# Performance work log

Hardware: AMD Instinct MI355X
Metric: run time of the kernel (lower is better)

Reference implementation:

```python
import jax, jax.numpy as jnp
import numpy as np

DIM = 192
NUM_HEADS = 4
B, H, W = 2, 256, 256
EPS = 1e-12  # torch F.normalize default eps


def setup_inputs() -> dict:
    key = jax.random.key(0)
    k1, k2, k3 = jax.random.split(key, 3)
    x = jax.random.normal(k1, (B, DIM, H, W), dtype=jnp.float32)
    # depthwise qkv conv: groups=DIM, each group maps 1 in-ch -> 3 out-ch; torch OIHW layout (3*DIM, 1, 3, 3)
    w_qkv = jax.random.normal(k2, (3 * DIM, 1, 3, 3), dtype=jnp.float32) * 0.1
    temperature = jnp.ones((NUM_HEADS, 1, 1), dtype=jnp.float32)
    # 1x1 projection conv, stored as [out, in]
    w_proj = jax.random.normal(k3, (DIM, DIM), dtype=jnp.float32) * (1.0 / np.sqrt(DIM))
    return {"x": x, "w_qkv": w_qkv, "temperature": temperature, "w_proj": w_proj}


def reference(x, w_qkv, temperature, w_proj):
    b, c, h, w = x.shape
    num_heads = temperature.shape[0]
    ch = c // num_heads  # channels per head
    # grouped (depthwise) 3x3 conv producing qkv; torch grouped-conv channel order
    # matches feature_group_count ordering (3 consecutive out-chs per group)... but
    # note torch chunk(3, dim=1) splits the 3*c output into contiguous thirds, so
    # q gets out-channels [0, c), etc. We replicate exactly with same layout.
    qkv = jax.lax.conv_general_dilated(
        x, w_qkv, window_strides=(1, 1), padding=((1, 1), (1, 1)),
        feature_group_count=c,
        dimension_numbers=("NCHW", "OIHW", "NCHW"))
    q, k, v = jnp.split(qkv, 3, axis=1)  # each [b, c, h, w]
    q = q.reshape(b, num_heads, ch, h * w)
    k = k.reshape(b, num_heads, ch, h * w)
    v = v.reshape(b, num_heads, ch, h * w)
    # L2 normalize along spatial dim (torch F.normalize with eps clamp)
    q = q / jnp.maximum(jnp.linalg.norm(q, axis=-1, keepdims=True), EPS)
    k = k / jnp.maximum(jnp.linalg.norm(k, axis=-1, keepdims=True), EPS)
    # channel-channel cosine attention, [b, head, ch, ch] (small)
    attn = jnp.einsum("bhcn,bhdn->bhcd", q, k) * temperature
    attn = jax.nn.softmax(attn, axis=-1)
    out = jnp.einsum("bhcd,bhdn->bhcn", attn, v).reshape(b, c, h, w)
    # 1x1 projection conv
    out = jnp.einsum("oi,bihw->bohw", w_proj, out)
    return out
```

## Files before the change

### kernel.cpp

```cpp
#include <hip/hip_runtime.h>
#include <math.h>

#define BB 2
#define CC 192
#define NH 4
#define CH 48
#define SRCP 16
#define HH 256
#define WW 256
#define NPIX (HH*WW)

typedef __attribute__((ext_vector_type(8))) short short8;
typedef __attribute__((ext_vector_type(4))) float f4;

static __device__ __forceinline__ unsigned short f2bf(float f) {
    union { float f; unsigned int u; } c; c.f = f;
    unsigned int r = c.u + 0x7fffu + ((c.u >> 16) & 1u);
    return (unsigned short)(r >> 16);
}

__global__ __launch_bounds__(256, 2) void k_conv(
    const float* __restrict__ x, const float* __restrict__ wqkv,
    unsigned short* __restrict__ vws, float* __restrict__ Sws,
    float* __restrict__ sqws)
{
    __shared__ float wlds[3*CH*9];
    __shared__ unsigned int qk32[2][CH][132];

    const int tid = threadIdx.x;
    const int hd = blockIdx.x;
    const int y  = blockIdx.y;
    const int b  = blockIdx.z;

    for (int i = tid; i < 3*CH*9; i += 256) {
        int type = i / (CH*9);
        int rem  = i - type*(CH*9);
        wlds[i] = wqkv[type*(CC*9) + hd*(CH*9) + rem];
    }
    __syncthreads();

    {
        const int xp = tid;
        const int y0 = (y > 0) ? (y-1) : 0;
        const int y2 = (y < HH-1) ? (y+1) : y;
        const int xl = (xp > 0) ? (xp-1) : 0;
        const int xr = (xp < WW-1) ? (xp+1) : xp;
        const float my0 = (y > 0) ? 1.f : 0.f;
        const float my2 = (y < HH-1) ? 1.f : 0.f;
        const float mx0 = (xp > 0) ? 1.f : 0.f;
        const float mx2 = (xp < WW-1) ? 1.f : 0.f;
        const float m00 = my0*mx0, m02 = my0*mx2, m20 = my2*mx0, m22 = my2*mx2;

        #pragma unroll
        for (int type = 0; type < 2; ++type) {
            const int srcbase = type*64 + SRCP*hd;
            const float* wt = &wlds[type*(CH*9)];
            for (int g = 0; g < SRCP; ++g) {
                const float* base = x + ((size_t)(b*CC + srcbase + g)*HH)*WW;
                const float* r0 = base + (size_t)y0*WW;
                const float* r1 = base + (size_t)y *WW;
                const float* r2 = base + (size_t)y2*WW;
                float a00 = r0[xl]*m00, a01 = r0[xp]*my0, a02 = r0[xr]*m02;
                float a10 = r1[xl]*mx0, a11 = r1[xp],     a12 = r1[xr]*mx2;
                float a20 = r2[xl]*m20, a21 = r2[xp]*my2, a22 = r2[xr]*m22;
                #pragma unroll
                for (int r = 0; r < 3; ++r) {
                    const int cl = 3*g + r;
                    const float* w = wt + cl*9;
                    float val = a00*w[0] + a01*w[1] + a02*w[2]
                              + a10*w[3] + a11*w[4] + a12*w[5]
                              + a20*w[6] + a21*w[7] + a22*w[8];
                    ((unsigned short*)&qk32[type][cl][0])[xp] = f2bf(val);
                }
            }
        }

        unsigned int vpack[24];
        {
            const int srcbase = 128 + SRCP*hd;
            const float* wt = &wlds[2*(CH*9)];
            #pragma unroll
            for (int g = 0; g < SRCP; ++g) {
                const float* base = x + ((size_t)(b*CC + srcbase + g)*HH)*WW;
                const float* r0 = base + (size_t)y0*WW;
                const float* r1 = base + (size_t)y *WW;
                const float* r2 = base + (size_t)y2*WW;
                float a00 = r0[xl]*m00, a01 = r0[xp]*my0, a02 = r0[xr]*m02;
                float a10 = r1[xl]*mx0, a11 = r1[xp],     a12 = r1[xr]*mx2;
                float a20 = r2[xl]*m20, a21 = r2[xp]*my2, a22 = r2[xr]*m22;
                #pragma unroll
                for (int r = 0; r < 3; ++r) {
                    const int cl = 3*g + r;
                    const float* w = wt + cl*9;
                    float val = a00*w[0] + a01*w[1] + a02*w[2]
                              + a10*w[3] + a11*w[4] + a12*w[5]
                              + a20*w[6] + a21*w[7] + a22*w[8];
                    unsigned int u = f2bf(val);
                    if (cl & 1) vpack[cl >> 1] |= (u << 16);
                    else        vpack[cl >> 1]  = u;
                }
            }
        }
        {
            unsigned short* vp = vws + ((size_t)b*NPIX + (size_t)y*WW + xp)*CC + hd*CH;
            #pragma unroll
            for (int st = 0; st < 6; ++st) {
                uint4 u; u.x = vpack[st*4+0]; u.y = vpack[st*4+1];
                         u.z = vpack[st*4+2]; u.w = vpack[st*4+3];
                *(uint4*)(vp + st*8) = u;
            }
        }
    }
    __syncthreads();

    if (tid < 2*CH) {
        const int which = tid / CH;
        const int cl = tid - which*CH;
        const uint4* row = (const uint4*)&qk32[which][cl][0];
        float ssum = 0.f;
        for (int j = 0; j < 32; ++j) {
            uint4 u = row[j];
            #pragma unroll
            for (int q4 = 0; q4 < 4; ++q4) {
                unsigned int w = (&u.x)[q4];
                float lo = __uint_as_float(w << 16);
                float hi = __uint_as_float(w & 0xffff0000u);
                ssum = fmaf(lo, lo, ssum);
                ssum = fmaf(hi, hi, ssum);
            }
        }
        atomicAdd(&sqws[((b*NH + hd)*2 + which)*CH + cl], ssum);
    }

    {
        const int lane = tid & 63;
        const int wv = tid >> 6;
        const int m = lane & 15, quad = lane >> 4;
        for (int p = wv; p < 9; p += 4) {
            const int ct = p / 3, dt = p - ct*3;
            f4 acc = {0.f, 0.f, 0.f, 0.f};
            const char* qbase = (const char*)&qk32[0][ct*16 + m][0] + quad*16;
            const char* kbase = (const char*)&qk32[1][dt*16 + m][0] + quad*16;
            #pragma unroll
            for (int ks = 0; ks < 8; ++ks) {
                short8 afr = *(const short8*)(qbase + ks*64);
                short8 bfr = *(const short8*)(kbase + ks*64);
                acc = __builtin_amdgcn_mfma_f32_16x16x32_bf16(afr, bfr, acc, 0, 0, 0);
            }
            const int c0 = ct*16 + quad*4, d = dt*16 + m;
            float* Sp = Sws + ((size_t)(b*NH + hd)*CH + c0)*CH + d;
            #pragma unroll
            for (int r = 0; r < 4; ++r) atomicAdd(Sp + r*CH, acc[r]);
        }
    }
}

__global__ __launch_bounds__(256) void k_attn(
    const float* __restrict__ Sws, const float* __restrict__ sqws,
    const float* __restrict__ temp, const float* __restrict__ wproj,
    unsigned short* __restrict__ W2bf)
{
    __shared__ float att[CH][CH+1];
    __shared__ float wp[CC][CH+1];
    __shared__ float nrm[2][CH];

    const int tid = threadIdx.x;
    const int b  = blockIdx.x >> 2;
    const int hd = blockIdx.x & 3;

    if (tid < 2*CH) {
        int which = tid / CH, cl = tid - which*CH;
        nrm[which][cl] = fmaxf(sqrtf(sqws[((b*NH + hd)*2 + which)*CH + cl]), 1e-12f);
    }
    __syncthreads();

    const float tscale = temp[hd];
    for (int m = tid; m < CH*CH; m += 256) {
        int c = m / CH, d = m - c*CH;
        att[c][d] = Sws[((size_t)(b*NH + hd)*CH + c)*CH + d] * tscale
                    / (nrm[0][c] * nrm[1][d]);
    }
    __syncthreads();

    if (tid < CH) {
        float mx = -1e30f;
        for (int d = 0; d < CH; ++d) mx = fmaxf(mx, att[tid][d]);
        float sm = 0.f;
        for (int d = 0; d < CH; ++d) { float e = expf(att[tid][d] - mx); att[tid][d] = e; sm += e; }
        float inv = 1.f / sm;
        for (int d = 0; d < CH; ++d) att[tid][d] *= inv;
    }

    for (int m = tid; m < CC*CH; m += 256) {
        int o = m / CH, il = m - o*CH;
        wp[o][il] = wproj[o*CC + hd*CH + il];
    }
    __syncthreads();

    const int o0  = (tid & 31) * 6;
    const int dl0 = (tid >> 5) * 6;
    float a[6][6];
    #pragma unroll
    for (int i = 0; i < 6; ++i)
        #pragma unroll
        for (int j = 0; j < 6; ++j) a[i][j] = 0.f;
    for (int il = 0; il < CH; ++il) {
        float wv[6], av[6];
        #pragma unroll
        for (int i = 0; i < 6; ++i) wv[i] = wp[o0+i][il];
        #pragma unroll
        for (int j = 0; j < 6; ++j) av[j] = att[il][dl0+j];
        #pragma unroll
        for (int i = 0; i < 6; ++i)
            #pragma unroll
            for (int j = 0; j < 6; ++j)
                a[i][j] = fmaf(wv[i], av[j], a[i][j]);
    }
    #pragma unroll
    for (int i = 0; i < 6; ++i)
        #pragma unroll
        for (int j = 0; j < 6; ++j)
            W2bf[((size_t)b*CC + o0 + i)*CC + hd*CH + dl0 + j] = f2bf(a[i][j]);
}

__global__ __launch_bounds__(256, 2) void k_out(
    const unsigned short* __restrict__ vws, const unsigned short* __restrict__ W2bf,
    float* __restrict__ out)
{
    __shared__ unsigned short w2l[CC][200];

    const int tid = threadIdx.x;
    const int b  = blockIdx.y;
    const int n0 = blockIdx.x * 128;

    {
        const uint4* src = (const uint4*)(W2bf + (size_t)b*CC*CC);
        for (int i = tid; i < CC*24; i += 256) {
            int o = i / 24, c = i - o*24;
            *(uint4*)&w2l[o][c*8] = src[i];
        }
    }
    __syncthreads();

    const int lane = tid & 63;
    const int wv = tid >> 6;
    const int m0  = (wv & 1) * 96;
    const int nn0 = (wv >> 1) * 64;
    const int m = lane & 15, quad = lane >> 4;

    f4 acc[6][4];
    #pragma unroll
    for (int mt = 0; mt < 6; ++mt)
        #pragma unroll
        for (int nt = 0; nt < 4; ++nt) acc[mt][nt] = (f4){0.f, 0.f, 0.f, 0.f};

    const unsigned short* vb = vws + ((size_t)b*NPIX + n0 + nn0 + m)*CC + quad*8;

    #pragma unroll
    for (int ks = 0; ks < 6; ++ks) {
        short8 bfr[4];
        #pragma unroll
        for (int nt = 0; nt < 4; ++nt)
            bfr[nt] = *(const short8*)(vb + (size_t)(nt*16)*CC + ks*32);
        short8 afr[6];
        #pragma unroll
        for (int mt = 0; mt < 6; ++mt)
            afr[mt] = *(const short8*)&w2l[m0 + mt*16 + m][ks*32 + quad*8];
        #pragma unroll
        for (int mt = 0; mt < 6; ++mt)
            #pragma unroll
            for (int nt = 0; nt < 4; ++nt)
                acc[mt][nt] = __builtin_amdgcn_mfma_f32_16x16x32_bf16(afr[mt], bfr[nt], acc[mt][nt], 0, 0, 0);
    }

    #pragma unroll
    for (int mt = 0; mt < 6; ++mt) {
        const int o = m0 + mt*16 + quad*4;
        #pragma unroll
        for (int nt = 0; nt < 4; ++nt) {
            const int px = n0 + nn0 + nt*16 + m;
            float* op = out + ((size_t)(b*CC + o))*NPIX + px;
            #pragma unroll
            for (int r = 0; r < 4; ++r) op[(size_t)r*NPIX] = acc[mt][nt][r];
        }
    }
}

extern "C" void kernel_launch(void* const* d_in, const int* in_sizes, int n_in,
                              void* d_out, int out_size, void* d_ws, size_t ws_size,
                              hipStream_t stream)
{
    const float* x     = (const float*)d_in[0];
    const float* wqkv  = (const float*)d_in[1];
    const float* temp  = (const float*)d_in[2];
    const float* wproj = (const float*)d_in[3];
    float* out = (float*)d_out;
    (void)in_sizes; (void)n_in; (void)out_size; (void)ws_size;

    unsigned short* vws = (unsigned short*)d_ws;
    const size_t VBYTES = (size_t)BB*CC*NPIX*sizeof(unsigned short);
    float* Sws  = (float*)((char*)d_ws + VBYTES);
    float* sqws = Sws + (size_t)BB*NH*CH*CH;
    unsigned short* W2bf = (unsigned short*)(sqws + (size_t)BB*NH*2*CH);

    hipMemsetAsync(Sws, 0, (size_t)(BB*NH*CH*CH + BB*NH*2*CH)*sizeof(float), stream);
    k_conv<<<dim3(NH, HH, BB), 256, 0, stream>>>(x, wqkv, vws, Sws, sqws);
    k_attn<<<dim3(BB*NH), 256, 0, stream>>>(Sws, sqws, temp, wproj, W2bf);
    k_out<<<dim3(NPIX/128, BB), 256, 0, stream>>>(vws, W2bf, out);
}
```

Before: 321.9 us.

## Split conv rows into half-width tiles with DPP neighbor exchange; drop LDS staging

The depthwise conv kernel now processes half a row per block, with the two thread halves covering different channel groups. Horizontal neighbors come from DPP lane shifts and readlane of halo values instead of three separate global loads per row. Weights are read straight from global memory rather than staged in LDS, and the output kernel reads W2 directly from global memory instead of copying it to LDS. This cuts redundant global loads and LDS footprint to raise occupancy, at the cost of twice as many atomic adds into the S accumulator and uncached weight reads.

```diff
diff --git a/kernel.cpp b/kernel.cpp
--- a/kernel.cpp
+++ b/kernel.cpp
@@ -5,7 +5,6 @@
 #define CC 192
 #define NH 4
 #define CH 48
-#define SRCP 16
 #define HH 256
 #define WW 256
 #define NPIX (HH*WW)
@@ -19,96 +18,107 @@
     return (unsigned short)(r >> 16);
 }
 
-__global__ __launch_bounds__(256, 2) void k_conv(
+template<int CTRL>
+static __device__ __forceinline__ float dppmv(float v) {
+    return __int_as_float(__builtin_amdgcn_update_dpp(
+        0, __float_as_int(v), CTRL, 0xf, 0xf, true));
+}
+#define WAVE_SHR1 0x138
+#define WAVE_SHL1 0x130
+
+static __device__ __forceinline__ float rdlane(float v, int l) {
+    return __int_as_float(__builtin_amdgcn_readlane(__float_as_int(v), l));
+}
+
+__global__ __launch_bounds__(256, 4) void k_conv(
     const float* __restrict__ x, const float* __restrict__ wqkv,
     unsigned short* __restrict__ vws, float* __restrict__ Sws,
     float* __restrict__ sqws)
 {
-    __shared__ float wlds[3*CH*9];
-    __shared__ unsigned int qk32[2][CH][132];
+    __shared__ unsigned int qk32[2][CH][72];
 
     const int tid = threadIdx.x;
     const int hd = blockIdx.x;
-    const int y  = blockIdx.y;
+    const int y  = blockIdx.y >> 1;
+    const int x0 = (blockIdx.y & 1) * 128;
     const int b  = blockIdx.z;
 
-    for (int i = tid; i < 3*CH*9; i += 256) {
-        int type = i / (CH*9);
-        int rem  = i - type*(CH*9);
-        wlds[i] = wqkv[type*(CC*9) + hd*(CH*9) + rem];
-    }
-    __syncthreads();
-
-    {
-        const int xp = tid;
-        const int y0 = (y > 0) ? (y-1) : 0;
-        const int y2 = (y < HH-1) ? (y+1) : y;
-        const int xl = (xp > 0) ? (xp-1) : 0;
-        const int xr = (xp < WW-1) ? (xp+1) : xp;
-        const float my0 = (y > 0) ? 1.f : 0.f;
-        const float my2 = (y < HH-1) ? 1.f : 0.f;
-        const float mx0 = (xp > 0) ? 1.f : 0.f;
-        const float mx2 = (xp < WW-1) ? 1.f : 0.f;
-        const float m00 = my0*mx0, m02 = my0*mx2, m20 = my2*mx0, m22 = my2*mx2;
-
-        #pragma unroll
-        for (int type = 0; type < 2; ++type) {
-            const int srcbase = type*64 + SRCP*hd;
-            const float* wt = &wlds[type*(CH*9)];
-            for (int g = 0; g < SRCP; ++g) {
-                const float* base = x + ((size_t)(b*CC + srcbase + g)*HH)*WW;
-                const float* r0 = base + (size_t)y0*WW;
-                const float* r1 = base + (size_t)y *WW;
-                const float* r2 = base + (size_t)y2*WW;
-                float a00 = r0[xl]*m00, a01 = r0[xp]*my0, a02 = r0[xr]*m02;
-                float a10 = r1[xl]*mx0, a11 = r1[xp],     a12 = r1[xr]*mx2;
-                float a20 = r2[xl]*m20, a21 = r2[xp]*my2, a22 = r2[xr]*m22;
-                #pragma unroll
-                for (int r = 0; r < 3; ++r) {
-                    const int cl = 3*g + r;
-                    const float* w = wt + cl*9;
-                    float val = a00*w[0] + a01*w[1] + a02*w[2]
-                              + a10*w[3] + a11*w[4] + a12*w[5]
-                              + a20*w[6] + a21*w[7] + a22*w[8];
-                    ((unsigned short*)&qk32[type][cl][0])[xp] = f2bf(val);
+    const int lane  = tid & 63;
+    const int chalf = tid >> 7;
+    const int lpx   = tid & 127;
+    const int xp    = x0 + lpx;
+    const int wstart = x0 + (((tid >> 6) & 1) << 6);
+
+    const int y0c = (y > 0) ? y-1 : 0;
+    const int y2c = (y < HH-1) ? y+1 : y;
+    const float m0 = (y > 0) ? 1.f : 0.f;
+    const float m2 = (y < HH-1) ? 1.f : 0.f;
+    const int ro0 = y0c*WW, ro1 = y*WW, ro2 = y2c*WW;
+
+    const int hrow = lane >> 1;
+    const int hside = lane & 1;
+    const int hx = hside ? (wstart + 64) : (wstart - 1);
+    const bool hact = (lane < 6) && (hx >= 0) && (hx < WW);
+    const int hoff = ((hrow == 0) ? ro0 : ((hrow == 1) ? ro1 : ro2)) + hx;
+    const float hmask = (hrow == 0) ? m0 : ((hrow == 2) ? m2 : 1.f);
+    const bool is0  = (lane == 0);
+    const bool is63 = (lane == 63);
+
+    unsigned int vpack[12];
+
+    #pragma unroll
+    for (int type = 0; type < 3; ++type) {
+        #pragma unroll
+        for (int gg = 0; gg < 8; ++gg) {
+            const int g  = chalf*8 + gg;
+            const int ic = type*64 + hd*16 + g;
+            const float* xch = x + ((size_t)(b*CC + ic))*NPIX;
+            const float* wp9 = wqkv + ((size_t)(type*CC + hd*CH + 3*g))*9;
+
+            float v0 = xch[ro0 + xp] * m0;
+            float v1 = xch[ro1 + xp];
+            float v2 = xch[ro2 + xp] * m2;
+            float hv = 0.f;
+            if (hact) hv = xch[hoff];
+            hv *= hmask;
+
+            float l0 = dppmv<WAVE_SHR1>(v0), r0 = dppmv<WAVE_SHL1>(v0);
+            float l1 = dppmv<WAVE_SHR1>(v1), r1 = dppmv<WAVE_SHL1>(v1);
+            float l2 = dppmv<WAVE_SHR1>(v2), r2 = dppmv<WAVE_SHL1>(v2);
+            float sL0 = rdlane(hv, 0), sR0 = rdlane(hv, 1);
+            float sL1 = rdlane(hv, 2), sR1 = rdlane(hv, 3);
+            float sL2 = rdlane(hv, 4), sR2 = rdlane(hv, 5);
+            l0 = is0 ? sL0 : l0;  r0 = is63 ? sR0 : r0;
+            l1 = is0 ? sL1 : l1;  r1 = is63 ? sR1 : r1;
+            l2 = is0 ? sL2 : l2;  r2 = is63 ? sR2 : r2;
+
+            #pragma unroll
+            for (int rr = 0; rr < 3; ++rr) {
+                const float* w = wp9 + rr*9;
+                float val = l0*w[0] + v0*w[1] + r0*w[2]
+                          + l1*w[3] + v1*w[4] + r1*w[5]
+                          + l2*w[6] + v2*w[7] + r2*w[8];
+                if (type == 2) {
+                    const int cll = 3*gg + rr;
+                    unsigned int u = f2bf(val);
+                    if (cll & 1) vpack[cll >> 1] |= (u << 16);
+                    else         vpack[cll >> 1]  = u;
+                } else {
+                    const int cl = 3*g + rr;
+                    ((unsigned short*)&qk32[type][cl][0])[lpx] = f2bf(val);
                 }
             }
         }
-
-        unsigned int vpack[24];
-        {
-            const int srcbase = 128 + SRCP*hd;
-            const float* wt = &wlds[2*(CH*9)];
-            #pragma unroll
-            for (int g = 0; g < SRCP; ++g) {
-                const float* base = x + ((size_t)(b*CC + srcbase + g)*HH)*WW;
-                const float* r0 = base + (size_t)y0*WW;
-                const float* r1 = base + (size_t)y *WW;
-                const float* r2 = base + (size_t)y2*WW;
-                float a00 = r0[xl]*m00, a01 = r0[xp]*my0, a02 = r0[xr]*m02;
-                float a10 = r1[xl]*mx0, a11 = r1[xp],     a12 = r1[xr]*mx2;
-                float a20 = r2[xl]*m20, a21 = r2[xp]*my2, a22 = r2[xr]*m22;
-                #pragma unroll
-                for (int r = 0; r < 3; ++r) {
-                    const int cl = 3*g + r;
-                    const float* w = wt + cl*9;
-                    float val = a00*w[0] + a01*w[1] + a02*w[2]
-                              + a10*w[3] + a11*w[4] + a12*w[5]
-                              + a20*w[6] + a21*w[7] + a22*w[8];
-                    unsigned int u = f2bf(val);
-                    if (cl & 1) vpack[cl >> 1] |= (u << 16);
-                    else        vpack[cl >> 1]  = u;
-                }
-            }
-        }
-        {
-            unsigned short* vp = vws + ((size_t)b*NPIX + (size_t)y*WW + xp)*CC + hd*CH;
-            #pragma unroll
-            for (int st = 0; st < 6; ++st) {
-                uint4 u; u.x = vpack[st*4+0]; u.y = vpack[st*4+1];
-                         u.z = vpack[st*4+2]; u.w = vpack[st*4+3];
-                *(uint4*)(vp + st*8) = u;
-            }
+    }
+
+    {
+        unsigned short* vp = vws + ((size_t)b*NPIX + (size_t)y*WW + xp)*CC
+                             + hd*CH + chalf*24;
+        #pragma unroll
+        for (int st = 0; st < 3; ++st) {
+            uint4 u; u.x = vpack[st*4+0]; u.y = vpack[st*4+1];
+                     u.z = vpack[st*4+2]; u.w = vpack[st*4+3];
+            *(uint4*)(vp + st*8) = u;
         }
     }
     __syncthreads();
@@ -118,7 +128,8 @@
         const int cl = tid - which*CH;
         const uint4* row = (const uint4*)&qk32[which][cl][0];
         float ssum = 0.f;
-        for (int j = 0; j < 32; ++j) {
+        #pragma unroll
+        for (int j = 0; j < 16; ++j) {
             uint4 u = row[j];
             #pragma unroll
             for (int q4 = 0; q4 < 4; ++q4) {
@@ -133,18 +144,17 @@
     }
 
     {
-        const int lane = tid & 63;
         const int wv = tid >> 6;
         const int m = lane & 15, quad = lane >> 4;
         for (int p = wv; p < 9; p += 4) {
             const int ct = p / 3, dt = p - ct*3;
             f4 acc = {0.f, 0.f, 0.f, 0.f};
-            const char* qbase = (const char*)&qk32[0][ct*16 + m][0] + quad*16;
-            const char* kbase = (const char*)&qk32[1][dt*16 + m][0] + quad*16;
-            #pragma unroll
-            for (int ks = 0; ks < 8; ++ks) {
-                short8 afr = *(const short8*)(qbase + ks*64);
-                short8 bfr = *(const short8*)(kbase + ks*64);
+            const char* qb = (const char*)&qk32[0][ct*16 + m][0] + quad*16;
+            const char* kb = (const char*)&qk32[1][dt*16 + m][0] + quad*16;
+            #pragma unroll
+            for (int ks = 0; ks < 4; ++ks) {
+                short8 afr = *(const short8*)(qb + ks*64);
+                short8 bfr = *(const short8*)(kb + ks*64);
                 acc = __builtin_amdgcn_mfma_f32_16x16x32_bf16(afr, bfr, acc, 0, 0, 0);
             }
             const int c0 = ct*16 + quad*4, d = dt*16 + m;
@@ -223,24 +233,13 @@
             W2bf[((size_t)b*CC + o0 + i)*CC + hd*CH + dl0 + j] = f2bf(a[i][j]);
 }
 
-__global__ __launch_bounds__(256, 2) void k_out(
+__global__ __launch_bounds__(256, 3) void k_out(
     const unsigned short* __restrict__ vws, const unsigned short* __restrict__ W2bf,
     float* __restrict__ out)
 {
-    __shared__ unsigned short w2l[CC][200];
-
     const int tid = threadIdx.x;
     const int b  = blockIdx.y;
     const int n0 = blockIdx.x * 128;
-
-    {
-        const uint4* src = (const uint4*)(W2bf + (size_t)b*CC*CC);
-        for (int i = tid; i < CC*24; i += 256) {
-            int o = i / 24, c = i - o*24;
-            *(uint4*)&w2l[o][c*8] = src[i];
-        }
-    }
-    __syncthreads();
 
     const int lane = tid & 63;
     const int wv = tid >> 6;
@@ -255,6 +254,7 @@
         for (int nt = 0; nt < 4; ++nt) acc[mt][nt] = (f4){0.f, 0.f, 0.f, 0.f};
 
     const unsigned short* vb = vws + ((size_t)b*NPIX + n0 + nn0 + m)*CC + quad*8;
+    const unsigned short* ab = W2bf + ((size_t)b*CC + m0 + m)*CC + quad*8;
 
     #pragma unroll
     for (int ks = 0; ks < 6; ++ks) {
@@ -265,7 +265,7 @@
         short8 afr[6];
         #pragma unroll
         for (int mt = 0; mt < 6; ++mt)
-            afr[mt] = *(const short8*)&w2l[m0 + mt*16 + m][ks*32 + quad*8];
+            afr[mt] = *(const short8*)(ab + (size_t)(mt*16)*CC + ks*32);
         #pragma unroll
         for (int mt = 0; mt < 6; ++mt)
             #pragma unroll
@@ -304,7 +304,7 @@
     unsigned short* W2bf = (unsigned short*)(sqws + (size_t)BB*NH*2*CH);
 
     hipMemsetAsync(Sws, 0, (size_t)(BB*NH*CH*CH + BB*NH*2*CH)*sizeof(float), stream);
-    k_conv<<<dim3(NH, HH, BB), 256, 0, stream>>>(x, wqkv, vws, Sws, sqws);
+    k_conv<<<dim3(NH, 2*HH, BB), 256, 0, stream>>>(x, wqkv, vws, Sws, sqws);
     k_attn<<<dim3(BB*NH), 256, 0, stream>>>(Sws, sqws, temp, wproj, W2bf);
     k_out<<<dim3(NPIX/128, BB), 256, 0, stream>>>(vws, W2bf, out);
 }
```

New measurement: 612.9 us. 90.4% more time.
